# Performance work log

Hardware: AMD Instinct MI355X
Metric: run time of the kernel (lower is better)

The kernel has to match this reference:

```python
import jax, jax.numpy as jnp
import numpy as np

NUM_GRAPHS = 128
N_NODES = 50000
N_EDGES = 400000
EMB = 384
L = 5
BN_EPS = 1e-5


def _bn(h, gamma, beta):
    # training-mode BatchNorm1d over the node/edge dim (biased variance, like torch)
    m = h.mean(axis=0)
    v = h.var(axis=0)
    return gamma * (h - m) * jax.lax.rsqrt(v + BN_EPS) + beta


def setup_inputs() -> dict:
    key = jax.random.key(0)
    ks = jax.random.split(key, 16)
    batch = jnp.sort(jax.random.randint(ks[0], (N_NODES,), 0, NUM_GRAPHS))
    x = jax.random.randint(ks[1], (N_NODES, 9), 0, 64)
    edge_index = jax.random.randint(ks[2], (2, N_EDGES), 0, N_NODES)
    edge_attr = jax.random.randint(ks[3], (N_EDGES, 3), 0, 8)
    s = 0.05
    atom_emb = jax.random.normal(ks[4], (9, 64, EMB), jnp.float32) * s
    bond_emb = jax.random.normal(ks[5], (3, 8, EMB), jnp.float32) * s
    # per-layer GINE MLP params, stacked over layers
    W1 = jax.random.normal(ks[6], (L, EMB, 2 * EMB), jnp.float32) * (1.0 / np.sqrt(EMB))
    b1 = jnp.zeros((L, 2 * EMB), jnp.float32)
    g1 = jnp.ones((L, 2 * EMB), jnp.float32)
    be1 = jnp.zeros((L, 2 * EMB), jnp.float32)
    W2 = jax.random.normal(ks[7], (L, 2 * EMB, EMB), jnp.float32) * (1.0 / np.sqrt(2 * EMB))
    b2 = jnp.zeros((L, EMB), jnp.float32)
    # outer per-layer BatchNorm params
    gbn = jnp.ones((L, EMB), jnp.float32)
    bbn = jnp.zeros((L, EMB), jnp.float32)
    return {"batch": batch, "x": x, "edge_index": edge_index, "edge_attr": edge_attr,
            "atom_emb": atom_emb, "bond_emb": bond_emb,
            "W1": W1, "b1": b1, "g1": g1, "be1": be1,
            "W2": W2, "b2": b2, "gbn": gbn, "bbn": bbn}


def reference(batch, x, edge_index, edge_attr, atom_emb, bond_emb,
              W1, b1, g1, be1, W2, b2, gbn, bbn):
    # AtomEncoder / BondEncoder: sum of per-column embedding lookups
    h = atom_emb[jnp.arange(9), x].sum(axis=1)          # [N, EMB]
    e = bond_emb[jnp.arange(3), edge_attr].sum(axis=1)  # [E, EMB]
    src, dst = edge_index[0], edge_index[1]
    for i in range(W1.shape[0]):
        # GINEConv: sum_j relu(x_j + e_ij)  (edge_weight defaults to ones)
        msg = jax.nn.relu(h[src] + e)                                   # [E, EMB]
        agg = jax.ops.segment_sum(msg, dst, num_segments=N_NODES)      # [N, EMB]
        z = h + agg                                                     # (1+eps)*x_i + agg, eps=0
        # MLP: Linear -> BN -> ReLU -> Linear
        z = z @ W1[i] + b1[i]
        z = jax.nn.relu(_bn(z, g1[i], be1[i]))
        z = z @ W2[i] + b2[i]
        # outer BN + ReLU (drop_ratio = 0.0)
        h = jax.nn.relu(_bn(z, gbn[i], bbn[i]))
    # standard pooling: global_add_pool
    graph_emb = jax.ops.segment_sum(h, batch, num_segments=NUM_GRAPHS)  # [G, EMB]
    return graph_emb, h
```

## Files before the change

### kernel.cpp

```cpp
#include <hip/hip_runtime.h>
#include <stdint.h>

#define NN 50000
#define NE 400000
#define EMB 384
#define NH 768
#define NL 5

typedef __bf16 bf16x8_t __attribute__((ext_vector_type(8)));
typedef float  f32x4_t  __attribute__((ext_vector_type(4)));

__device__ __forceinline__ float bflo(uint32_t u){ union{uint32_t u;float f;} v; v.u = u<<16; return v.f; }
__device__ __forceinline__ float bfhi(uint32_t u){ union{uint32_t u;float f;} v; v.u = u & 0xffff0000u; return v.f; }
__device__ __forceinline__ uint16_t f2bf(float f){
  union{float f;uint32_t u;} v; v.f=f;
  uint32_t r = v.u + 0x7fffu + ((v.u>>16)&1u);
  return (uint16_t)(r>>16);
}
__device__ __forceinline__ uint32_t bfpack2(float a, float b){
  return (uint32_t)f2bf(a) | ((uint32_t)f2bf(b)<<16);
}
__device__ __forceinline__ uint32_t bfpack2h(float a, float b){
  uint32_t r;
  asm("v_cvt_pk_bf16_f32 %0, %1, %2" : "=v"(r) : "v"(a), "v"(b));
  return r;
}
__device__ __forceinline__ bf16x8_t as_bf16x8(uint4 u){
  union{uint4 a; bf16x8_t b;} c; c.a = u; return c.b;
}

__device__ __forceinline__ void gld16(uint16_t* ldsp, const uint16_t* gp){
  __builtin_amdgcn_global_load_lds(
      (const __attribute__((address_space(1))) uint32_t*)gp,
      (__attribute__((address_space(3))) uint32_t*)ldsp,
      16, 0, 0);
}

__global__ void hist_kernel(const int* __restrict__ dst, int* __restrict__ count){
  int i = blockIdx.x*256 + threadIdx.x;
  if (i < NE) atomicAdd(&count[dst[i]], 1);
}
__global__ void scan_block_sum(const int* __restrict__ count, int* __restrict__ bsum, int n){
  __shared__ int s[256];
  int i = blockIdx.x*256 + threadIdx.x;
  s[threadIdx.x] = (i<n) ? count[i] : 0;
  __syncthreads();
  for (int st=128; st>0; st>>=1){
    if (threadIdx.x < st) s[threadIdx.x] += s[threadIdx.x+st];
    __syncthreads();
  }
  if (threadIdx.x==0) bsum[blockIdx.x] = s[0];
}
__global__ void scan_excl_small(int* __restrict__ bsum, int nb){
  __shared__ int s[256];
  int t = threadIdx.x;
  int v = (t<nb) ? bsum[t] : 0;
  s[t] = v;
  __syncthreads();
  for (int st=1; st<256; st<<=1){
    int u = (t>=st) ? s[t-st] : 0;
    __syncthreads();
    s[t] += u;
    __syncthreads();
  }
  if (t<nb) bsum[t] = s[t] - v;
}
__global__ void scan_final(const int* __restrict__ count, const int* __restrict__ bsum,
                           int* __restrict__ rowptr, int* __restrict__ cursor, int n){
  __shared__ int s[256];
  int t = threadIdx.x;
  int i = blockIdx.x*256 + t;
  int v = (i<n) ? count[i] : 0;
  s[t] = v;
  __syncthreads();
  for (int st=1; st<256; st<<=1){
    int u = (t>=st) ? s[t-st] : 0;
    __syncthreads();
    s[t] += u;
    __syncthreads();
  }
  int off = bsum[blockIdx.x] + s[t] - v;
  if (i < n){
    rowptr[i] = off; cursor[i] = off;
    if (i == n-1) rowptr[n] = off + v;
  }
}
__global__ void scatter_kernel(const int* __restrict__ dst, const int* __restrict__ src,
                               const int* __restrict__ eattr, int* __restrict__ cursor,
                               int* __restrict__ csr_src, int* __restrict__ csr_code){
  int e = blockIdx.x*256 + threadIdx.x;
  if (e < NE){
    int p = atomicAdd(&cursor[dst[e]], 1);
    csr_src[p] = src[e];
    csr_code[p] = eattr[e*3] | (eattr[e*3+1]<<3) | (eattr[e*3+2]<<6);
  }
}

__global__ void build_bond(const float* __restrict__ bemb, uint16_t* __restrict__ bt){
  const int code = blockIdx.x;
  const int t0 = code&7, t1=(code>>3)&7, t2=code>>6;
  const int c = threadIdx.x;
  const float2 a = ((const float2*)(bemb + (size_t)( 0+t0)*EMB))[c];
  const float2 b = ((const float2*)(bemb + (size_t)( 8+t1)*EMB))[c];
  const float2 d = ((const float2*)(bemb + (size_t)(16+t2)*EMB))[c];
  ((uint32_t*)(bt + (size_t)code*EMB))[c] = bfpack2(a.x+b.x+d.x, a.y+b.y+d.y);
}

__global__ void transpose_w(const float* __restrict__ in, uint16_t* __restrict__ outp,
                            int R, int Cc){
  __shared__ float tile[32][33];
  const size_t lo = (size_t)blockIdx.z * R * Cc;
  int cb = blockIdx.x*32, rb = blockIdx.y*32;
  int r = rb + threadIdx.y, c = cb + threadIdx.x;
  if (r < R && c < Cc) tile[threadIdx.y][threadIdx.x] = in[lo + (size_t)r*Cc + c];
  __syncthreads();
  int orr = cb + threadIdx.y, occ = rb + threadIdx.x;
  if (orr < Cc && occ < R) outp[lo + (size_t)orr*R + occ] = f2bf(tile[threadIdx.x][threadIdx.y]);
}

__global__ __launch_bounds__(256) void atom_encode(
    const int* __restrict__ x, const float* __restrict__ aemb,
    uint16_t* __restrict__ h){
  const int w = threadIdx.x >> 6, lane = threadIdx.x & 63;
  const int i = blockIdx.x*4 + w;
  if (i >= NN) return;
  float a0=0,a1=0,a2=0,a3=0,a4=0,a5=0;
  #pragma unroll
  for (int k=0;k<9;k++){
    const int idx = x[i*9+k];
    const float2* p = (const float2*)(aemb + ((size_t)(k*64+idx))*EMB) + lane*3;
    float2 u0=p[0], u1=p[1], u2=p[2];
    a0+=u0.x; a1+=u0.y; a2+=u1.x; a3+=u1.y; a4+=u2.x; a5+=u2.y;
  }
  uint32_t* hp = (uint32_t*)(h + (size_t)i*EMB) + lane*3;
  hp[0]=bfpack2(a0,a1); hp[1]=bfpack2(a2,a3); hp[2]=bfpack2(a4,a5);
}

template<int BNREL>
__global__ __launch_bounds__(256) void agg_kernel(
    const uint16_t* __restrict__ in, const uint16_t* __restrict__ bondt,
    const float* __restrict__ scale, const float* __restrict__ shift,
    const int* __restrict__ rowptr, const int* __restrict__ csr_src,
    const int* __restrict__ csr_code, uint16_t* __restrict__ za){
  const int w = threadIdx.x >> 6, lane = threadIdx.x & 63;
  const int i = blockIdx.x*4 + w;
  if (i >= NN) return;

  float sc0=0,sc1=0,sc2=0,sc3=0,sc4=0,sc5=0, sh0=0,sh1=0,sh2=0,sh3=0,sh4=0,sh5=0;
  if (BNREL){
    const int c = lane*6;
    sc0=scale[c]; sc1=scale[c+1]; sc2=scale[c+2]; sc3=scale[c+3]; sc4=scale[c+4]; sc5=scale[c+5];
    sh0=shift[c]; sh1=shift[c+1]; sh2=shift[c+2]; sh3=shift[c+3]; sh4=shift[c+4]; sh5=shift[c+5];
  }

  const uint32_t* hs = (const uint32_t*)(in + (size_t)i*EMB) + lane*3;
  uint32_t s0=hs[0], s1=hs[1], s2=hs[2];
  float a0,a1,a2,a3,a4,a5;
  if (BNREL){
    a0 = fmaxf(bflo(s0)*sc0+sh0, 0.f); a1 = fmaxf(bfhi(s0)*sc1+sh1, 0.f);
    a2 = fmaxf(bflo(s1)*sc2+sh2, 0.f); a3 = fmaxf(bfhi(s1)*sc3+sh3, 0.f);
    a4 = fmaxf(bflo(s2)*sc4+sh4, 0.f); a5 = fmaxf(bfhi(s2)*sc5+sh5, 0.f);
  } else {
    a0 = bflo(s0); a1 = bfhi(s0); a2 = bflo(s1); a3 = bfhi(s1); a4 = bflo(s2); a5 = bfhi(s2);
  }

  const int rs = rowptr[i], re = rowptr[i+1];
  int k = rs;
  for (; k + 4 <= re; k += 4){
    int sj[4], cj[4];
    #pragma unroll
    for (int j=0;j<4;j++){ sj[j]=csr_src[k+j]; cj[j]=csr_code[k+j]; }
    uint32_t u[4][3], b[4][3];
    #pragma unroll
    for (int j=0;j<4;j++){
      const uint32_t* hp = (const uint32_t*)(in + (size_t)sj[j]*EMB) + lane*3;
      u[j][0]=hp[0]; u[j][1]=hp[1]; u[j][2]=hp[2];
      const uint32_t* bp = (const uint32_t*)(bondt + (size_t)cj[j]*EMB) + lane*3;
      b[j][0]=bp[0]; b[j][1]=bp[1]; b[j][2]=bp[2];
    }
    #pragma unroll
    for (int j=0;j<4;j++){
      float v0,v1,v2,v3,v4,v5;
      if (BNREL){
        v0 = fmaxf(bflo(u[j][0])*sc0+sh0, 0.f); v1 = fmaxf(bfhi(u[j][0])*sc1+sh1, 0.f);
        v2 = fmaxf(bflo(u[j][1])*sc2+sh2, 0.f); v3 = fmaxf(bfhi(u[j][1])*sc3+sh3, 0.f);
        v4 = fmaxf(bflo(u[j][2])*sc4+sh4, 0.f); v5 = fmaxf(bfhi(u[j][2])*sc5+sh5, 0.f);
      } else {
        v0=bflo(u[j][0]); v1=bfhi(u[j][0]); v2=bflo(u[j][1]);
        v3=bfhi(u[j][1]); v4=bflo(u[j][2]); v5=bfhi(u[j][2]);
      }
      a0 += fmaxf(v0+bflo(b[j][0]), 0.f); a1 += fmaxf(v1+bfhi(b[j][0]), 0.f);
      a2 += fmaxf(v2+bflo(b[j][1]), 0.f); a3 += fmaxf(v3+bfhi(b[j][1]), 0.f);
      a4 += fmaxf(v4+bflo(b[j][2]), 0.f); a5 += fmaxf(v5+bfhi(b[j][2]), 0.f);
    }
  }
  for (; k < re; k++){
    const int s = csr_src[k];
    const int code = csr_code[k];
    const uint32_t* hp = (const uint32_t*)(in + (size_t)s*EMB) + lane*3;
    uint32_t u0=hp[0], u1=hp[1], u2=hp[2];
    const uint32_t* bp = (const uint32_t*)(bondt + (size_t)code*EMB) + lane*3;
    uint32_t b0=bp[0], b1=bp[1], b2=bp[2];
    float v0,v1,v2,v3,v4,v5;
    if (BNREL){
      v0 = fmaxf(bflo(u0)*sc0+sh0, 0.f); v1 = fmaxf(bfhi(u0)*sc1+sh1, 0.f);
      v2 = fmaxf(bflo(u1)*sc2+sh2, 0.f); v3 = fmaxf(bfhi(u1)*sc3+sh3, 0.f);
      v4 = fmaxf(bflo(u2)*sc4+sh4, 0.f); v5 = fmaxf(bfhi(u2)*sc5+sh5, 0.f);
    } else {
      v0=bflo(u0); v1=bfhi(u0); v2=bflo(u1); v3=bfhi(u1); v4=bflo(u2); v5=bfhi(u2);
    }
    a0 += fmaxf(v0+bflo(b0), 0.f); a1 += fmaxf(v1+bfhi(b0), 0.f);
    a2 += fmaxf(v2+bflo(b1), 0.f); a3 += fmaxf(v3+bfhi(b1), 0.f);
    a4 += fmaxf(v4+bflo(b2), 0.f); a5 += fmaxf(v5+bfhi(b2), 0.f);
  }

  uint32_t* zp = (uint32_t*)(za + (size_t)i*EMB) + lane*3;
  zp[0] = bfpack2(a0,a1);
  zp[1] = bfpack2(a2,a3);
  zp[2] = bfpack2(a4,a5);
}

template<int BNA, int KK>
__global__ __launch_bounds__(256, 4) void gemm_bt(
    const uint16_t* __restrict__ A, const uint16_t* __restrict__ Bt,
    const float* __restrict__ bias, const float* __restrict__ scA,
    const float* __restrict__ shA, uint16_t* __restrict__ C,
    float* __restrict__ stats, int M, int N, int nbr){
  constexpr int NK = KK/32;
  constexpr int NPART = NK/2;
  __shared__ __align__(16) uint16_t panel[2][2][4096];
  __shared__ float sAs[BNA ? KK : 1];
  __shared__ float hAs[BNA ? KK : 1];
  __shared__ float csum[128];
  __shared__ float csq[128];

  const int tid = threadIdx.x;
  const int nbc = N >> 7;
  const int xcd = blockIdx.x & 7;
  const int slot = blockIdx.x >> 3;
  const int bcol = slot % nbc;
  const int brow = (slot / nbc)*8 + xcd;
  if (brow >= nbr) return;
  const int rowbase = brow << 7;

  const int lane = tid & 63;
  const int w = tid >> 6;
  const int quad = lane >> 4, l16 = lane & 15;

  const int s0 = tid, s1 = 256 + tid;
  const int r0 = s0 & 127, r1 = s1 & 127;
  const int pb0 = bcol*128 + (r0 & 64) + ((r0 & 15) << 2) + ((r0 >> 4) & 3);
  const int pb1 = bcol*128 + (r1 & 64) + ((r1 & 15) << 2) + ((r1 >> 4) & 3);
  const uint16_t* gB0 = Bt + (size_t)pb0*KK + (s0>>7)*8;
  const uint16_t* gB1 = Bt + (size_t)pb1*KK + (s1>>7)*8;

  int rowA0 = rowbase + w*32 + l16;      if (rowA0 >= M) rowA0 = M-1;
  int rowA1 = rowbase + w*32 + 16 + l16; if (rowA1 >= M) rowA1 = M-1;
  const uint16_t* gA0 = A + (size_t)rowA0*KK + quad*8;
  const uint16_t* gA1 = A + (size_t)rowA1*KK + quad*8;

  if (BNA){
    for (int i = tid; i < KK; i += 256){ sAs[i] = scA[i]; hAs[i] = shA[i]; }
  }

  f32x4_t acc[2][2][4];
  #pragma unroll
  for (int mi=0;mi<2;mi++)
    #pragma unroll
    for (int g=0;g<2;g++)
      #pragma unroll
      for (int nj=0;nj<4;nj++)
        acc[mi][g][nj] = (f32x4_t){0.f,0.f,0.f,0.f};

  uint4 ar0[4], ar1[4];

  gld16(&panel[0][0][s0*8], gB0);
  gld16(&panel[0][0][s1*8], gB1);
  gld16(&panel[0][1][s0*8], gB0 + 32);
  gld16(&panel[0][1][s1*8], gB1 + 32);
  ar0[0] = *(const uint4*)(gA0);      ar1[0] = *(const uint4*)(gA1);
  ar0[1] = *(const uint4*)(gA0 + 32); ar1[1] = *(const uint4*)(gA1 + 32);
  __syncthreads();

  #pragma unroll
  for (int p = 0; p < NPART; ++p){
    if (p + 1 < NPART){
      const int kf = (p+1)*2;
      gld16(&panel[(p+1)&1][0][s0*8], gB0 + kf*32);
      gld16(&panel[(p+1)&1][0][s1*8], gB1 + kf*32);
      gld16(&panel[(p+1)&1][1][s0*8], gB0 + (kf+1)*32);
      gld16(&panel[(p+1)&1][1][s1*8], gB1 + (kf+1)*32);
      ar0[kf&3]     = *(const uint4*)(gA0 + kf*32);
      ar1[kf&3]     = *(const uint4*)(gA1 + kf*32);
      ar0[(kf+1)&3] = *(const uint4*)(gA0 + (kf+1)*32);
      ar1[(kf+1)&3] = *(const uint4*)(gA1 + (kf+1)*32);
    }
    #pragma unroll
    for (int s = 0; s < 2; ++s){
      const int kq = p*2 + s;
      const uint4 ca0 = ar0[kq&3];
      const uint4 ca1 = ar1[kq&3];
      bf16x8_t fa0, fa1;
      if (BNA){
        const int kb = kq*32 + quad*8;
        float4 sv0 = *(const float4*)&sAs[kb];
        float4 sv1 = *(const float4*)&sAs[kb+4];
        float4 hv0 = *(const float4*)&hAs[kb];
        float4 hv1 = *(const float4*)&hAs[kb+4];
        float e0,e1,e2,e3,e4,e5,e6,e7;
        e0=fmaxf(bflo(ca0.x)*sv0.x+hv0.x,0.f); e1=fmaxf(bfhi(ca0.x)*sv0.y+hv0.y,0.f);
        e2=fmaxf(bflo(ca0.y)*sv0.z+hv0.z,0.f); e3=fmaxf(bfhi(ca0.y)*sv0.w+hv0.w,0.f);
        e4=fmaxf(bflo(ca0.z)*sv1.x+hv1.x,0.f); e5=fmaxf(bfhi(ca0.z)*sv1.y+hv1.y,0.f);
        e6=fmaxf(bflo(ca0.w)*sv1.z+hv1.z,0.f); e7=fmaxf(bfhi(ca0.w)*sv1.w+hv1.w,0.f);
        fa0 = as_bf16x8(make_uint4(bfpack2h(e0,e1),bfpack2h(e2,e3),bfpack2h(e4,e5),bfpack2h(e6,e7)));
        e0=fmaxf(bflo(ca1.x)*sv0.x+hv0.x,0.f); e1=fmaxf(bfhi(ca1.x)*sv0.y+hv0.y,0.f);
        e2=fmaxf(bflo(ca1.y)*sv0.z+hv0.z,0.f); e3=fmaxf(bfhi(ca1.y)*sv0.w+hv0.w,0.f);
        e4=fmaxf(bflo(ca1.z)*sv1.x+hv1.x,0.f); e5=fmaxf(bfhi(ca1.z)*sv1.y+hv1.y,0.f);
        e6=fmaxf(bflo(ca1.w)*sv1.z+hv1.z,0.f); e7=fmaxf(bfhi(ca1.w)*sv1.w+hv1.w,0.f);
        fa1 = as_bf16x8(make_uint4(bfpack2h(e0,e1),bfpack2h(e2,e3),bfpack2h(e4,e5),bfpack2h(e6,e7)));
      } else {
        fa0 = as_bf16x8(ca0);
        fa1 = as_bf16x8(ca1);
      }
      #pragma unroll
      for (int g=0; g<2; ++g)
        #pragma unroll
        for (int nj=0; nj<4; ++nj){
          bf16x8_t fb = *(const bf16x8_t*)&panel[p&1][s][(quad*128 + g*64 + nj*16 + l16)*8];
          acc[0][g][nj] = __builtin_amdgcn_mfma_f32_16x16x32_bf16(fa0, fb, acc[0][g][nj], 0,0,0);
          acc[1][g][nj] = __builtin_amdgcn_mfma_f32_16x16x32_bf16(fa1, fb, acc[1][g][nj], 0,0,0);
        }
    }
    __syncthreads();
  }

  if (tid < 128){ csum[tid]=0.f; csq[tid]=0.f; }
  __syncthreads();

  const int colbase = bcol*128 + l16*4;
  float bv[2][4], ssum[2][4], sq[2][4];
  #pragma unroll
  for (int g=0;g<2;g++)
    #pragma unroll
    for (int nj=0;nj<4;nj++){
      bv[g][nj] = bias[colbase + g*64 + nj];
      ssum[g][nj] = 0.f; sq[g][nj] = 0.f;
    }

  #pragma unroll
  for (int mi=0;mi<2;mi++){
    #pragma unroll
    for (int r=0;r<4;r++){
      const int grow = rowbase + w*32 + mi*16 + quad*4 + r;
      if (grow < M){
        #pragma unroll
        for (int g=0;g<2;g++){
          float v0 = acc[mi][g][0][r] + bv[g][0];
          float v1 = acc[mi][g][1][r] + bv[g][1];
          float v2 = acc[mi][g][2][r] + bv[g][2];
          float v3 = acc[mi][g][3][r] + bv[g][3];
          uint2 pk = make_uint2(bfpack2h(v0,v1), bfpack2h(v2,v3));
          *(uint2*)(C + (size_t)grow*N + colbase + g*64) = pk;
          ssum[g][0]+=v0; ssum[g][1]+=v1; ssum[g][2]+=v2; ssum[g][3]+=v3;
          sq[g][0]+=v0*v0; sq[g][1]+=v1*v1; sq[g][2]+=v2*v2; sq[g][3]+=v3*v3;
        }
      }
    }
  }
  #pragma unroll
  for (int g=0;g<2;g++)
    #pragma unroll
    for (int nj=0;nj<4;nj++){
      ssum[g][nj] += __shfl_xor(ssum[g][nj], 16); ssum[g][nj] += __shfl_xor(ssum[g][nj], 32);
      sq[g][nj]   += __shfl_xor(sq[g][nj],   16); sq[g][nj]   += __shfl_xor(sq[g][nj],   32);
    }
  if (quad == 0){
    #pragma unroll
    for (int g=0;g<2;g++)
      #pragma unroll
      for (int nj=0;nj<4;nj++){
        atomicAdd(&csum[g*64 + l16*4 + nj], ssum[g][nj]);
        atomicAdd(&csq [g*64 + l16*4 + nj], sq[g][nj]);
      }
  }
  __syncthreads();
  if (tid < 128){
    atomicAdd(&stats[bcol*128 + tid], csum[tid]);
    atomicAdd(&stats[N + bcol*128 + tid], csq[tid]);
  }
}

__global__ void bn_finalize(float* __restrict__ stats, const float* __restrict__ gamma,
                            const float* __restrict__ beta, float* __restrict__ scale,
                            float* __restrict__ shift, int n, float invM){
  int c = blockIdx.x*256 + threadIdx.x;
  if (c < n){
    float mean = stats[c]*invM;
    float var  = stats[n+c]*invM - mean*mean;
    float sc = gamma[c] * rsqrtf(var + 1e-5f);
    scale[c] = sc;
    shift[c] = beta[c] - mean*sc;
    stats[c] = 0.f;
    stats[n+c] = 0.f;
  }
}

__global__ void bn_relu_final(const uint16_t* __restrict__ u, const float* __restrict__ scale,
                              const float* __restrict__ shift, float* __restrict__ hf){
  int i = blockIdx.x*256 + threadIdx.x;
  const int total2 = NN*EMB/2;
  if (i >= total2) return;
  uint32_t v = ((const uint32_t*)u)[i];
  int c = (i*2) % EMB;
  float f0 = fmaxf(bflo(v)*scale[c  ] + shift[c  ], 0.f);
  float f1 = fmaxf(bfhi(v)*scale[c+1] + shift[c+1], 0.f);
  ((float2*)hf)[i] = make_float2(f0, f1);
}

__global__ void pool_kernel(const float* __restrict__ h, const int* __restrict__ batch,
                            float* __restrict__ pool){
  __shared__ int bs[64];
  int c = threadIdx.x;
  int n0 = blockIdx.x*64;
  if (c < 64){ int i = n0 + c; bs[c] = (i < NN) ? batch[i] : -1; }
  __syncthreads();
  float sum = 0.f; int cur = -1;
  for (int tt=0; tt<64; tt++){
    int i = n0 + tt;
    if (i >= NN) break;
    int g = bs[tt];
    float v = h[(size_t)i*EMB + c];
    if (g != cur){
      if (cur >= 0) atomicAdd(&pool[(size_t)cur*EMB + c], sum);
      cur = g; sum = v;
    } else sum += v;
  }
  if (cur >= 0) atomicAdd(&pool[(size_t)cur*EMB + c], sum);
}
__global__ void pool_to_out(const float* __restrict__ pool, float* __restrict__ outp){
  int i = blockIdx.x*256 + threadIdx.x;
  if (i < 128*EMB) outp[i] = pool[i];
}

extern "C" void kernel_launch(void* const* d_in, const int* in_sizes, int n_in,
                              void* d_out, int out_size, void* d_ws, size_t ws_size,
                              hipStream_t stream){
  (void)in_sizes; (void)n_in; (void)out_size; (void)ws_size;
  const int* batch = (const int*)d_in[0];
  const int* x     = (const int*)d_in[1];
  const int* eidx  = (const int*)d_in[2];
  const int* eattr = (const int*)d_in[3];
  const float* aemb = (const float*)d_in[4];
  const float* bemb = (const float*)d_in[5];
  const float* W1 = (const float*)d_in[6];
  const float* b1 = (const float*)d_in[7];
  const float* g1 = (const float*)d_in[8];
  const float* be1= (const float*)d_in[9];
  const float* W2 = (const float*)d_in[10];
  const float* b2 = (const float*)d_in[11];
  const float* gbn= (const float*)d_in[12];
  const float* bbn= (const float*)d_in[13];
  float* out = (float*)d_out;

  char* base = (char*)d_ws;
  size_t off = 0;
  auto alloc = [&](size_t bytes) -> void* {
    void* p = base + off;
    off = (off + bytes + 255) & ~(size_t)255;
    return p;
  };
  uint16_t* za   = (uint16_t*)alloc((size_t)NN*EMB*2);
  uint16_t* zm   = (uint16_t*)alloc((size_t)NN*EMB*2);
  uint16_t* t    = (uint16_t*)alloc((size_t)NN*NH*2);
  uint16_t* W1t  = (uint16_t*)alloc((size_t)NL*NH*EMB*2);
  uint16_t* W2t  = (uint16_t*)alloc((size_t)NL*EMB*NH*2);
  uint16_t* bondt= (uint16_t*)alloc((size_t)512*EMB*2);
  float* stats1  = (float*)alloc(NH*2*4);
  float* stats2  = (float*)alloc(EMB*2*4);
  float* scale1  = (float*)alloc(NH*4);
  float* shift1  = (float*)alloc(NH*4);
  float* scale2  = (float*)alloc(EMB*4);
  float* shift2  = (float*)alloc(EMB*4);
  float* pool    = (float*)alloc(128*EMB*4);
  int* count   = (int*)alloc((size_t)NN*4);
  int* rowptr  = (int*)alloc((size_t)(NN+1)*4);
  int* cursor  = (int*)alloc((size_t)NN*4);
  int* bsum    = (int*)alloc(256*4);
  int* csr_src = (int*)alloc((size_t)NE*4);
  int* csr_code= (int*)alloc((size_t)NE*4);

  const int* esrc = eidx;
  const int* edst = eidx + NE;
  const int nsb = (NN + 255)/256;

  hipMemsetAsync(count, 0, (size_t)NN*4, stream);
  hist_kernel<<<(NE+255)/256, 256, 0, stream>>>(edst, count);
  scan_block_sum<<<nsb, 256, 0, stream>>>(count, bsum, NN);
  scan_excl_small<<<1, 256, 0, stream>>>(bsum, nsb);
  scan_final<<<nsb, 256, 0, stream>>>(count, bsum, rowptr, cursor, NN);
  scatter_kernel<<<(NE+255)/256, 256, 0, stream>>>(edst, esrc, eattr, cursor, csr_src, csr_code);

  build_bond<<<512, 192, 0, stream>>>(bemb, bondt);
  transpose_w<<<dim3(NH/32, EMB/32, NL), dim3(32,32), 0, stream>>>(W1, W1t, EMB, NH);
  transpose_w<<<dim3(EMB/32, NH/32, NL), dim3(32,32), 0, stream>>>(W2, W2t, NH, EMB);

  atom_encode<<<NN/4, 256, 0, stream>>>(x, aemb, zm);
  hipMemsetAsync(pool, 0, (size_t)128*EMB*4, stream);
  hipMemsetAsync(stats1, 0, (size_t)(6144 + 3072), stream);

  const int nbr = (NN + 127)/128;
  const int nbrr = ((nbr + 7)/8)*8;
  const int g1blocks = nbrr*(NH/128);
  const int g2blocks = nbrr*(EMB/128);
  for (int l = 0; l < NL; l++){
    if (l == 0)
      agg_kernel<0><<<NN/4, 256, 0, stream>>>(zm, bondt, nullptr, nullptr,
                                              rowptr, csr_src, csr_code, za);
    else
      agg_kernel<1><<<NN/4, 256, 0, stream>>>(zm, bondt, scale2, shift2,
                                              rowptr, csr_src, csr_code, za);
    gemm_bt<0, EMB><<<g1blocks, 256, 0, stream>>>(
        za, W1t + (size_t)l*NH*EMB, b1 + l*NH, nullptr, nullptr, t, stats1, NN, NH, nbr);
    bn_finalize<<<(NH+255)/256, 256, 0, stream>>>(stats1, g1 + l*NH, be1 + l*NH,
                                                  scale1, shift1, NH, 1.0f/NN);
    gemm_bt<1, NH><<<g2blocks, 256, 0, stream>>>(
        t, W2t + (size_t)l*EMB*NH, b2 + l*EMB, scale1, shift1, zm, stats2, NN, EMB, nbr);
    bn_finalize<<<(EMB+255)/256, 256, 0, stream>>>(stats2, gbn + l*EMB, bbn + l*EMB,
                                                   scale2, shift2, EMB, 1.0f/NN);
  }
  bn_relu_final<<<(NN*EMB/2 + 255)/256, 256, 0, stream>>>(zm, scale2, shift2, out + 128*EMB);
  pool_kernel<<<(NN+63)/64, 384, 0, stream>>>(out + 128*EMB, batch, pool);
  pool_to_out<<<(128*EMB+255)/256, 256, 0, stream>>>(pool, out);
}
```

Measured before the change: 1.306 ms.

## Stage B tiles through registers with XOR-swizzled LDS writes instead of direct-to-LDS loads

Replaces global_load_lds direct-to-LDS copies of the B panel with vectorized global loads into registers, prefetched two stages ahead and then written to LDS. The writes use an XOR swizzle, with a matching swizzled read index in the MFMA loop, to avoid LDS bank conflicts. The coalescing pattern also changes, since each group of 8 threads now reads a contiguous 128-byte span of a B column. The cost is more registers for the staging buffers, which may lower occupancy.

Result: slower. 1.544 ms (+18.2%).

```diff
diff --git a/kernel.cpp b/kernel.cpp
--- a/kernel.cpp
+++ b/kernel.cpp
@@ -27,13 +27,6 @@
 }
 __device__ __forceinline__ bf16x8_t as_bf16x8(uint4 u){
   union{uint4 a; bf16x8_t b;} c; c.a = u; return c.b;
-}
-
-__device__ __forceinline__ void gld16(uint16_t* ldsp, const uint16_t* gp){
-  __builtin_amdgcn_global_load_lds(
-      (const __attribute__((address_space(1))) uint32_t*)gp,
-      (__attribute__((address_space(3))) uint32_t*)ldsp,
-      16, 0, 0);
 }
 
 __global__ void hist_kernel(const int* __restrict__ dst, int* __restrict__ count){
@@ -247,21 +240,37 @@
   const int w = tid >> 6;
   const int quad = lane >> 4, l16 = lane & 15;
 
-  const int s0 = tid, s1 = 256 + tid;
-  const int r0 = s0 & 127, r1 = s1 & 127;
-  const int pb0 = bcol*128 + (r0 & 64) + ((r0 & 15) << 2) + ((r0 >> 4) & 3);
-  const int pb1 = bcol*128 + (r1 & 64) + ((r1 & 15) << 2) + ((r1 >> 4) & 3);
-  const uint16_t* gB0 = Bt + (size_t)pb0*KK + (s0>>7)*8;
-  const uint16_t* gB1 = Bt + (size_t)pb1*KK + (s1>>7)*8;
-
   int rowA0 = rowbase + w*32 + l16;      if (rowA0 >= M) rowA0 = M-1;
   int rowA1 = rowbase + w*32 + 16 + l16; if (rowA1 >= M) rowA1 = M-1;
   const uint16_t* gA0 = A + (size_t)rowA0*KK + quad*8;
   const uint16_t* gA1 = A + (size_t)rowA1*KK + quad*8;
 
+  const int bcol128 = bcol*128;
+
   if (BNA){
     for (int i = tid; i < KK; i += 256){ sAs[i] = scA[i]; hAs[i] = shA[i]; }
   }
+
+  auto loadB = [&](uint4* dst, int k0){
+    #pragma unroll
+    for (int c = 0; c < 4; ++c){
+      const int gidx = c*256 + tid;
+      const int col  = gidx >> 3;
+      const int koff = (gidx & 7) << 3;
+      dst[c] = *(const uint4*)(Bt + (size_t)(bcol128 + col)*KK + k0 + koff);
+    }
+  };
+  auto dswB = [&](int buf, const uint4* src){
+    #pragma unroll
+    for (int c = 0; c < 4; ++c){
+      const int gidx = c*256 + tid;
+      const int col  = gidx >> 3;
+      const int sx   = gidx & 7;
+      const int slab = sx >> 2, q = sx & 3;
+      const int rinv = (col & 64) | ((col & 3) << 4) | ((col >> 2) & 15);
+      *(uint4*)&panel[buf][slab][(q*128 + (rinv ^ sx))*8] = src[c];
+    }
+  };
 
   f32x4_t acc[2][2][4];
   #pragma unroll
@@ -272,24 +281,29 @@
       for (int nj=0;nj<4;nj++)
         acc[mi][g][nj] = (f32x4_t){0.f,0.f,0.f,0.f};
 
+  const int l16x0 = l16 ^ quad;
+  const int l16x1 = l16 ^ (4 + quad);
+
   uint4 ar0[4], ar1[4];
-
-  gld16(&panel[0][0][s0*8], gB0);
-  gld16(&panel[0][0][s1*8], gB1);
-  gld16(&panel[0][1][s0*8], gB0 + 32);
-  gld16(&panel[0][1][s1*8], gB1 + 32);
+  uint4 bq0[4], bq1[4];
+
+  loadB(bq0, 0);
+  if (NPART > 1) loadB(bq1, 64);
   ar0[0] = *(const uint4*)(gA0);      ar1[0] = *(const uint4*)(gA1);
   ar0[1] = *(const uint4*)(gA0 + 32); ar1[1] = *(const uint4*)(gA1 + 32);
+  dswB(0, bq0);
   __syncthreads();
 
   #pragma unroll
   for (int p = 0; p < NPART; ++p){
     if (p + 1 < NPART){
+      if ((p+1) & 1) dswB(1, bq1); else dswB(0, bq0);
+    }
+    if (p + 2 < NPART){
+      if ((p+2) & 1) loadB(bq1, (p+2)*64); else loadB(bq0, (p+2)*64);
+    }
+    if (p + 1 < NPART){
       const int kf = (p+1)*2;
-      gld16(&panel[(p+1)&1][0][s0*8], gB0 + kf*32);
-      gld16(&panel[(p+1)&1][0][s1*8], gB1 + kf*32);
-      gld16(&panel[(p+1)&1][1][s0*8], gB0 + (kf+1)*32);
-      gld16(&panel[(p+1)&1][1][s1*8], gB1 + (kf+1)*32);
       ar0[kf&3]     = *(const uint4*)(gA0 + kf*32);
       ar1[kf&3]     = *(const uint4*)(gA1 + kf*32);
       ar0[(kf+1)&3] = *(const uint4*)(gA0 + (kf+1)*32);
@@ -322,11 +336,12 @@
         fa0 = as_bf16x8(ca0);
         fa1 = as_bf16x8(ca1);
       }
+      const int lx = s ? l16x1 : l16x0;
       #pragma unroll
       for (int g=0; g<2; ++g)
         #pragma unroll
         for (int nj=0; nj<4; ++nj){
-          bf16x8_t fb = *(const bf16x8_t*)&panel[p&1][s][(quad*128 + g*64 + nj*16 + l16)*8];
+          bf16x8_t fb = *(const bf16x8_t*)&panel[p&1][s][(quad*128 + g*64 + nj*16 + lx)*8];
           acc[0][g][nj] = __builtin_amdgcn_mfma_f32_16x16x32_bf16(fa0, fb, acc[0][g][nj], 0,0,0);
           acc[1][g][nj] = __builtin_amdgcn_mfma_f32_16x16x32_bf16(fa1, fb, acc[1][g][nj], 0,0,0);
         }
@@ -337,7 +352,7 @@
   if (tid < 128){ csum[tid]=0.f; csq[tid]=0.f; }
   __syncthreads();
 
-  const int colbase = bcol*128 + l16*4;
+  const int colbase = bcol128 + l16*4;
   float bv[2][4], ssum[2][4], sq[2][4];
   #pragma unroll
   for (int g=0;g<2;g++)
@@ -385,8 +400,8 @@
   }
   __syncthreads();
   if (tid < 128){
-    atomicAdd(&stats[bcol*128 + tid], csum[tid]);
-    atomicAdd(&stats[N + bcol*128 + tid], csq[tid]);
+    atomicAdd(&stats[bcol128 + tid], csum[tid]);
+    atomicAdd(&stats[N + bcol128 + tid], csq[tid]);
   }
 }
 
```
